# Performance work log

Measured on AMD Instinct MI355X. Metric: run time of the kernel, lower is better.

## Reference

```python
import jax, jax.numpy as jnp
import numpy as np

B, N, M, D, HEADS, L, DFF, TSTEPS = 8, 1024, 512, 128, 8, 6, 512, 100
S = N + M
HD = D // HEADS


def _layer_norm(x, g, b):
    mu = jnp.mean(x, axis=-1, keepdims=True)
    var = jnp.var(x, axis=-1, keepdims=True)
    return (x - mu) * jax.lax.rsqrt(var + 1e-5) * g + b


def setup_inputs() -> dict:
    rng = np.random.default_rng(0)
    # sparse parity-check matrix, ~6 ones per check row
    H = (rng.random((M, N)) < 6.0 / N).astype(np.float32)
    # create_mask with n_rings=1: eye(S) plus variable<->check Tanner edges
    conn = np.eye(S, dtype=np.float32)
    conn[N:, :N] = np.maximum(conn[N:, :N], H)
    conn[:N, N:] = np.maximum(conn[:N, N:], H.T)
    mask = ~(conn > 0)  # True = attention blocked (src_mask semantics)

    key = jax.random.key(0)
    ks = jax.random.split(key, 16)
    s = 0.05  # weight init scale ~ 1/sqrt(d_model)
    return {
        "r_t": jax.random.normal(ks[0], (B, N), jnp.float32),
        "t": jax.random.randint(ks[1], (B,), 0, TSTEPS),
        "pcm": jnp.asarray(H.astype(np.int32)),
        "mask": jnp.asarray(mask),
        "src_embed": jax.random.uniform(ks[2], (S, D), jnp.float32),
        "time_table": jax.random.normal(ks[3], (TSTEPS, D), jnp.float32),
        "Wq": jax.random.normal(ks[4], (L, D, D), jnp.float32) * s,
        "Wk": jax.random.normal(ks[5], (L, D, D), jnp.float32) * s,
        "Wv": jax.random.normal(ks[6], (L, D, D), jnp.float32) * s,
        "Wo": jax.random.normal(ks[7], (L, D, D), jnp.float32) * s,
        "W1": jax.random.normal(ks[8], (L, D, DFF), jnp.float32) * s,
        "W2": jax.random.normal(ks[9], (L, DFF, D), jnp.float32) * s,
        "g1": jnp.ones((L, D), jnp.float32),
        "b1": jnp.zeros((L, D), jnp.float32),
        "g2": jnp.ones((L, D), jnp.float32),
        "b2": jnp.zeros((L, D), jnp.float32),
        "fc_w": jax.random.normal(ks[10], (D, 1), jnp.float32) * s,
        "fc_b": jnp.zeros((1,), jnp.float32),
    }


def reference(r_t, t, pcm, mask, src_embed, time_table, Wq, Wk, Wv, Wo,
              W1, W2, g1, b1, g2, b2, fc_w, fc_b):
    # to_bin: BPSK sign -> bit {0,1}
    bits = 0.5 * (1.0 - jnp.sign(r_t))                       # [B, N]
    syn = (bits @ pcm.T.astype(jnp.float32)) % 2.0           # mod-2 syndrome [B, M]
    nodes = jnp.concatenate([jnp.abs(r_t), syn], axis=-1)    # [B, S]
    x = src_embed[None, :, :] * nodes[:, :, None]            # [B, S, D]
    te = time_table[t]                                       # [B, D] time embedding
    x = te[:, None, :] * x                                   # time-modulated input
    bias = jnp.where(mask, -1e9, 0.0)[None, None]            # [1, 1, S, S]
    inv_sqrt_hd = 1.0 / jnp.sqrt(jnp.float32(HD))
    for l in range(L):
        h = _layer_norm(x, g1[l], b1[l])
        q = (h @ Wq[l]).reshape(B, S, HEADS, HD)
        k = (h @ Wk[l]).reshape(B, S, HEADS, HD)
        v = (h @ Wv[l]).reshape(B, S, HEADS, HD)
        scores = jnp.einsum('bqhd,bkhd->bhqk', q, k) * inv_sqrt_hd + bias
        p = jax.nn.softmax(scores, axis=-1)
        o = jnp.einsum('bhqk,bkhd->bqhd', p, v).reshape(B, S, D)
        x = x + o @ Wo[l]
        # FiLM-style time conditioning on the FFN branch
        h2 = _layer_norm(x, g2[l], b2[l]) * te[:, None, :]
        x = x + jax.nn.relu(h2 @ W1[l]) @ W2[l]
    return x @ fc_w + fc_b                                   # z_hat [B, S, 1]
```

## Files before the change

kernel.cpp:

```cpp
#include <hip/hip_runtime.h>
#include <cmath>
#include <cstdint>

constexpr int B_ = 8, N_ = 1024, M_ = 512, D_ = 128, S_ = 1536, L_ = 6, DFF_ = 512;
constexpr int ROWS = B_ * S_;
constexpr int MAXDEG = 64;
constexpr int LKEY = 32;
constexpr int RPB  = 48;
constexpr int NBLK = ROWS / RPB;
constexpr int BPB  = S_ / RPB;
constexpr int NTILE = 12;
constexpr int TILE  = 128 * 128;

typedef __bf16 bf16x8 __attribute__((ext_vector_type(8)));
typedef float  f32x4  __attribute__((ext_vector_type(4)));
typedef unsigned short u16x8 __attribute__((ext_vector_type(8)));

__device__ inline unsigned short f2bf(float f) {
  unsigned u = __float_as_uint(f);
  u += 0x7fffu + ((u >> 16) & 1u);
  return (unsigned short)(u >> 16);
}
__device__ inline float bf2f(unsigned short u) {
  return __uint_as_float(((unsigned)u) << 16);
}
__device__ inline void ull2f4(unsigned long long u, float* f) {
  f[0] = bf2f((unsigned short)(u));
  f[1] = bf2f((unsigned short)(u >> 16));
  f[2] = bf2f((unsigned short)(u >> 32));
  f[3] = bf2f((unsigned short)(u >> 48));
}

__device__ __forceinline__ void async_ld16(const unsigned short* g, unsigned short* l) {
  __builtin_amdgcn_global_load_lds(
      (const __attribute__((address_space(1))) unsigned int*)(uintptr_t)g,
      (__attribute__((address_space(3))) unsigned int*)(unsigned)(uintptr_t)l,
      16, 0, 0);
}
__device__ __forceinline__ void issue_tile(const unsigned short* tp, unsigned short* bs,
                                           int w, int lane) {
  for (int c = w; c < 32; c += 6)
    async_ld16(tp + c * 512 + lane * 8, bs + c * 512);
}

__global__ void adj_init(int* __restrict__ adj, int* __restrict__ adjcnt) {
  int s = blockIdx.x * blockDim.x + threadIdx.x;
  if (s < S_) { adj[s * MAXDEG] = s; adjcnt[s] = 1; }
}
__global__ void adj_build(const int* __restrict__ pcm, int* __restrict__ adj,
                          int* __restrict__ adjcnt) {
  int c = blockIdx.x;
  int lane = threadIdx.x;
  const int* row = pcm + c * N_;
  for (int base = 0; base < N_; base += 64) {
    int k = base + lane;
    if (row[k] != 0) {
      int s1 = atomicAdd(&adjcnt[N_ + c], 1);
      if (s1 < MAXDEG) adj[(N_ + c) * MAXDEG + s1] = k;
      int s2 = atomicAdd(&adjcnt[k], 1);
      if (s2 < MAXDEG) adj[k * MAXDEG + s2] = N_ + c;
    }
  }
}

__global__ void xinit_kernel(const float* __restrict__ r_t, const int* __restrict__ adj,
                             const int* __restrict__ adjcnt, const float* __restrict__ se,
                             const int* __restrict__ tt, const float* __restrict__ table,
                             float* __restrict__ x, unsigned* __restrict__ barrier_cnt) {
  int bs = blockIdx.x;
  int b = bs / S_, s = bs % S_;
  int d = threadIdx.x;
  if (bs < 8 && d == 0)
    __hip_atomic_store(barrier_cnt + bs * 32, 0u, __ATOMIC_RELAXED, __HIP_MEMORY_SCOPE_AGENT);
  float node;
  if (s < N_) {
    node = fabsf(r_t[b * N_ + s]);
  } else {
    int cnt = adjcnt[s]; cnt = cnt < MAXDEG ? cnt : MAXDEG;
    float sum = 0.f;
    for (int j = 0; j < cnt; ++j) {
      int k = adj[s * MAXDEG + j];
      if (k < N_) {
        float r = r_t[b * N_ + k];
        sum += (r < 0.f) ? 1.f : (r > 0.f ? 0.f : 0.5f);
      }
    }
    node = fmodf(sum, 2.0f);
  }
  x[(size_t)bs * D_ + d] = table[tt[b] * D_ + d] * se[s * D_ + d] * node;
}

constexpr int WLAYER = NTILE * TILE;

__global__ void wconv_kernel(const float* __restrict__ Wq, const float* __restrict__ Wk,
                             const float* __restrict__ Wv, const float* __restrict__ Wo,
                             const float* __restrict__ W1, const float* __restrict__ W2,
                             unsigned short* __restrict__ out) {
  __shared__ unsigned short tl[128 * 130];
  int bid = blockIdx.x;
  int l = bid / NTILE, tile = bid % NTILE;
  const float* src;
  int rstride, coff = 0;
  if (tile == 0)      { src = Wk + (size_t)l * D_ * D_;  rstride = D_; }
  else if (tile == 1) { src = Wv + (size_t)l * D_ * D_;  rstride = D_; }
  else if (tile == 2) { src = Wq + (size_t)l * D_ * D_;  rstride = D_; }
  else if (tile == 3) { src = Wo + (size_t)l * D_ * D_;  rstride = D_; }
  else {
    int c = (tile - 4) >> 1;
    if (((tile - 4) & 1) == 0) { src = W1 + (size_t)l * D_ * DFF_; rstride = DFF_; coff = c * 128; }
    else                       { src = W2 + (size_t)l * DFF_ * D_ + (size_t)c * 128 * D_; rstride = D_; }
  }
  for (int i = threadIdx.x; i < 16384; i += 256) {
    int kd = i >> 7, rr = i & 127;
    tl[kd * 130 + rr] = f2bf(src[(size_t)kd * rstride + coff + rr]);
  }
  __syncthreads();
  unsigned short* o = out + (size_t)bid * TILE;
  for (int i = threadIdx.x; i < 16384; i += 256) {
    int rr = i >> 7;
    int sw = (i >> 3) & 15, e = i & 7;
    int kd = (sw ^ (rr & 15)) * 8 + e;
    o[i] = tl[kd * 130 + rr];
  }
}

__device__ __forceinline__ void mfma4(const unsigned short* As, const unsigned short* Bs,
                                      int rowbase, int colbase, int quad, int l16,
                                      f32x4 (&acc)[4]) {
#pragma unroll
  for (int kk = 0; kk < 4; ++kk) {
    int cb = kk * 4 + quad;
    int row = rowbase + l16;
    bf16x8 a = __builtin_bit_cast(bf16x8, *(const uint4*)&As[row * 128 + ((cb ^ (row & 15)) << 3)]);
    bf16x8 bb[4];
#pragma unroll
    for (int ct = 0; ct < 4; ++ct) {
      int n = colbase + ct * 16 + l16;
      bb[ct] = __builtin_bit_cast(bf16x8, *(const uint4*)&Bs[n * 128 + ((cb ^ (n & 15)) << 3)]);
    }
#pragma unroll
    for (int ct = 0; ct < 4; ++ct)
      acc[ct] = __builtin_amdgcn_mfma_f32_16x16x32_bf16(a, bb[ct], acc[ct], 0, 0, 0);
  }
}

__device__ __forceinline__ void grid_barrier(unsigned* cnt, unsigned target) {
  __syncthreads();
  if (threadIdx.x == 0) {
    __hip_atomic_fetch_add(cnt, 1u, __ATOMIC_RELAXED, __HIP_MEMORY_SCOPE_AGENT);
    while (__hip_atomic_load(cnt, __ATOMIC_RELAXED, __HIP_MEMORY_SCOPE_AGENT) < target)
      __builtin_amdgcn_s_sleep(4);
  }
  __syncthreads();
}

__global__ void __launch_bounds__(384) mega_kernel(
    const float* __restrict__ x0, unsigned short* __restrict__ kv0,
    unsigned short* __restrict__ kv1, const unsigned short* __restrict__ wbf,
    const float* __restrict__ g1, const float* __restrict__ b1,
    const float* __restrict__ g2, const float* __restrict__ b2,
    const int* __restrict__ tt, const float* __restrict__ table,
    const int* __restrict__ adj, const int* __restrict__ adjc,
    const float* __restrict__ fcw, const float* __restrict__ fcb,
    float* __restrict__ out, unsigned* barrier_cnt) {
  __shared__ unsigned short As[RPB * 128];
  __shared__ unsigned short Bs[2][TILE];
  __shared__ unsigned short Cs[RPB * 128];
  __shared__ unsigned short KVs[RPB * 256];
  __shared__ float red1[2][RPB], red2[2][RPB];
  __shared__ int sKeys[RPB * LKEY];
  __shared__ int sCnt[RPB];
  const int row0 = blockIdx.x * RPB;
  const int b = row0 / S_;
  const int bS = b * S_;
  const int t = threadIdx.x, w = t >> 6, lane = t & 63, quad = lane >> 4, l16 = lane & 15;
  const int wr = w >> 1, wc = w & 1;
  const int rowbase = wr * 16, colbase = wc * 64;
  const int tbase = tt[b] * D_;
  unsigned* bcnt = barrier_cnt + b * 32;

  issue_tile(wbf, Bs[0], w, lane);

  f32x4 xreg[4];
#pragma unroll
  for (int ct = 0; ct < 4; ++ct)
#pragma unroll
    for (int i = 0; i < 4; ++i) {
      int row = row0 + rowbase + quad * 4 + i;
      int col = colbase + ct * 16 + l16;
      xreg[ct][i] = x0[(size_t)row * D_ + col];
    }
  if (t < RPB) {
    int c = adjc[row0 + t - bS];
    sCnt[t] = c < MAXDEG ? c : MAXDEG;
  }
  for (int i = t; i < RPB * LKEY; i += 384) {
    int r = i / LKEY, j = i % LKEY;
    sKeys[i] = adj[(row0 + r - bS) * MAXDEG + j];
  }

  for (int l = 0; l < L_; ++l) {
    const unsigned short* wt = wbf + (size_t)l * WLAYER;
    const float* g1l = g1 + l * D_;
    const float* b1l = b1 + l * D_;
    const float* g2l = g2 + l * D_;
    const float* b2l = b2 + l * D_;
    unsigned short* kv = (l & 1) ? kv1 : kv0;

    float mu1[4], rs1[4];
#pragma unroll
    for (int i = 0; i < 4; ++i) {
      float s = xreg[0][i] + xreg[1][i] + xreg[2][i] + xreg[3][i];
      for (int off = 1; off < 16; off <<= 1) s += __shfl_xor(s, off);
      if (l16 == 0) red1[wc][rowbase + quad * 4 + i] = s;
    }
    __syncthreads();
#pragma unroll
    for (int i = 0; i < 4; ++i) {
      int r = rowbase + quad * 4 + i;
      mu1[i] = (red1[0][r] + red1[1][r]) * (1.f / 128.f);
      float sq = 0.f;
#pragma unroll
      for (int ct = 0; ct < 4; ++ct) { float d = xreg[ct][i] - mu1[i]; sq += d * d; }
      for (int off = 1; off < 16; off <<= 1) sq += __shfl_xor(sq, off);
      if (l16 == 0) red2[wc][r] = sq;
    }
    __syncthreads();
#pragma unroll
    for (int i = 0; i < 4; ++i) {
      int r = rowbase + quad * 4 + i;
      rs1[i] = rsqrtf((red2[0][r] + red2[1][r]) * (1.f / 128.f) + 1e-5f);
    }
#pragma unroll
    for (int ct = 0; ct < 4; ++ct)
#pragma unroll
      for (int i = 0; i < 4; ++i) {
        int rowL = rowbase + quad * 4 + i;
        int col = colbase + ct * 16 + l16;
        float h = (xreg[ct][i] - mu1[i]) * rs1[i] * g1l[col] + b1l[col];
        As[rowL * 128 + (((col >> 3) ^ (rowL & 15)) << 3) + (col & 7)] = f2bf(h);
      }
    __syncthreads();

    issue_tile(wt + 1 * TILE, Bs[1], w, lane);
    {
      f32x4 acc[4];
#pragma unroll
      for (int j = 0; j < 4; ++j) acc[j] = f32x4{0.f, 0.f, 0.f, 0.f};
      mfma4(As, Bs[0], rowbase, colbase, quad, l16, acc);
#pragma unroll
      for (int ct = 0; ct < 4; ++ct)
#pragma unroll
        for (int i = 0; i < 4; ++i) {
          int rowL = rowbase + quad * 4 + i;
          KVs[rowL * 256 + colbase + ct * 16 + l16] = f2bf(acc[ct][i]);
        }
    }
    __syncthreads();
    issue_tile(wt + 2 * TILE, Bs[0], w, lane);
    {
      f32x4 acc[4];
#pragma unroll
      for (int j = 0; j < 4; ++j) acc[j] = f32x4{0.f, 0.f, 0.f, 0.f};
      mfma4(As, Bs[1], rowbase, colbase, quad, l16, acc);
#pragma unroll
      for (int ct = 0; ct < 4; ++ct)
#pragma unroll
        for (int i = 0; i < 4; ++i) {
          int rowL = rowbase + quad * 4 + i;
          KVs[rowL * 256 + 128 + colbase + ct * 16 + l16] = f2bf(acc[ct][i]);
        }
    }
    __syncthreads();
    issue_tile(wt + 3 * TILE, Bs[1], w, lane);
    {
      f32x4 acc[4];
#pragma unroll
      for (int j = 0; j < 4; ++j) acc[j] = f32x4{0.f, 0.f, 0.f, 0.f};
      mfma4(As, Bs[0], rowbase, colbase, quad, l16, acc);
#pragma unroll
      for (int ct = 0; ct < 4; ++ct)
#pragma unroll
        for (int i = 0; i < 4; ++i) {
          int rowL = rowbase + quad * 4 + i;
          int col = colbase + ct * 16 + l16;
          Cs[rowL * 128 + (((col >> 3) ^ (rowL & 15)) << 3) + (col & 7)] = f2bf(acc[ct][i]);
        }
    }
    for (int i = t; i < RPB * 128; i += 384) {
      int rL = i >> 7, cw = i & 127;
      unsigned u = *(const unsigned*)&KVs[rL * 256 + cw * 2];
      __hip_atomic_store((unsigned*)&kv[(size_t)(row0 + rL) * 256 + cw * 2],
                         u, __ATOMIC_RELAXED, __HIP_MEMORY_SCOPE_AGENT);
    }

    grid_barrier(bcnt, (unsigned)(BPB * (l + 1)));

    issue_tile(wt + 4 * TILE, Bs[0], w, lane);

    {
      const int rL = t >> 3, h = t & 7;
      const int s = row0 + rL - bS;
      const int cnt = sCnt[rL];
      float q[16];
      {
        u16x8 qa = *(const u16x8*)&Cs[rL * 128 + (((2 * h) ^ (rL & 15)) << 3)];
        u16x8 qb = *(const u16x8*)&Cs[rL * 128 + (((2 * h + 1) ^ (rL & 15)) << 3)];
#pragma unroll
        for (int j = 0; j < 8; ++j) { q[j] = bf2f(qa[j]); q[8 + j] = bf2f(qb[j]); }
      }
      float m = -1e30f, lsum = 0.f;
      float o16[16];
#pragma unroll
      for (int j = 0; j < 16; ++j) o16[j] = 0.f;
      for (int jb = 0; jb < cnt; jb += 4) {
        unsigned long long K[4][4], V[4][4];
#pragma unroll
        for (int u = 0; u < 4; ++u) {
          int j = jb + u;
          int key = 0;
          if (j < cnt) key = (j < LKEY) ? sKeys[rL * LKEY + j] : adj[s * MAXDEG + j];
          const unsigned long long* kp =
              (const unsigned long long*)(kv + (size_t)(bS + key) * 256 + h * 16);
#pragma unroll
          for (int c = 0; c < 4; ++c) {
            K[u][c] = __hip_atomic_load(kp + c, __ATOMIC_RELAXED, __HIP_MEMORY_SCOPE_AGENT);
            V[u][c] = __hip_atomic_load(kp + 32 + c, __ATOMIC_RELAXED, __HIP_MEMORY_SCOPE_AGENT);
          }
        }
#pragma unroll
        for (int u = 0; u < 4; ++u) {
          float kf[16], vf[16];
#pragma unroll
          for (int c = 0; c < 4; ++c) { ull2f4(K[u][c], kf + 4 * c); ull2f4(V[u][c], vf + 4 * c); }
          float dot = 0.f;
#pragma unroll
          for (int j = 0; j < 16; ++j) dot = fmaf(q[j], kf[j], dot);
          dot *= 0.25f;
          if (jb + u >= cnt) dot = -1e30f;
          const float mn = fmaxf(m, dot);
          const float rescale = __expf(m - mn);
          const float e = __expf(dot - mn);
          lsum = lsum * rescale + e;
#pragma unroll
          for (int j = 0; j < 16; ++j) o16[j] = o16[j] * rescale + e * vf[j];
          m = mn;
        }
      }
      const float inv = 1.f / lsum;
      u16x8 pk0, pk1;
#pragma unroll
      for (int j = 0; j < 8; ++j) {
        pk0[j] = f2bf(o16[j] * inv);
        pk1[j] = f2bf(o16[8 + j] * inv);
      }
      *(u16x8*)&As[rL * 128 + (((2 * h) ^ (rL & 15)) << 3)] = pk0;
      *(u16x8*)&As[rL * 128 + (((2 * h + 1) ^ (rL & 15)) << 3)] = pk1;
    }
    __syncthreads();

    f32x4 acc1[4];
#pragma unroll
    for (int j = 0; j < 4; ++j) acc1[j] = f32x4{0.f, 0.f, 0.f, 0.f};
    mfma4(As, Bs[1], rowbase, colbase, quad, l16, acc1);
    f32x4 xp[4];
#pragma unroll
    for (int ct = 0; ct < 4; ++ct)
#pragma unroll
      for (int i = 0; i < 4; ++i) xp[ct][i] = xreg[ct][i] + acc1[ct][i];
#pragma unroll
    for (int i = 0; i < 4; ++i) {
      float s = xp[0][i] + xp[1][i] + xp[2][i] + xp[3][i];
      for (int off = 1; off < 16; off <<= 1) s += __shfl_xor(s, off);
      if (l16 == 0) red1[wc][rowbase + quad * 4 + i] = s;
    }
    __syncthreads();
    float mu_[4], rs_[4];
#pragma unroll
    for (int i = 0; i < 4; ++i) {
      int r = rowbase + quad * 4 + i;
      mu_[i] = (red1[0][r] + red1[1][r]) * (1.f / 128.f);
      float sq = 0.f;
#pragma unroll
      for (int ct = 0; ct < 4; ++ct) { float d = xp[ct][i] - mu_[i]; sq += d * d; }
      for (int off = 1; off < 16; off <<= 1) sq += __shfl_xor(sq, off);
      if (l16 == 0) red2[wc][r] = sq;
    }
    __syncthreads();
#pragma unroll
    for (int i = 0; i < 4; ++i) {
      int r = rowbase + quad * 4 + i;
      rs_[i] = rsqrtf((red2[0][r] + red2[1][r]) * (1.f / 128.f) + 1e-5f);
    }
#pragma unroll
    for (int ct = 0; ct < 4; ++ct)
#pragma unroll
      for (int i = 0; i < 4; ++i) {
        int rowL = rowbase + quad * 4 + i;
        int col = colbase + ct * 16 + l16;
        float h2 = (xp[ct][i] - mu_[i]) * rs_[i] * g2l[col] + b2l[col];
        h2 *= table[tbase + col];
        As[rowL * 128 + (((col >> 3) ^ (rowL & 15)) << 3) + (col & 7)] = f2bf(h2);
      }
    __syncthreads();

    f32x4 acc2[4];
#pragma unroll
    for (int j = 0; j < 4; ++j) acc2[j] = f32x4{0.f, 0.f, 0.f, 0.f};
    for (int c = 0; c < 4; ++c) {
      issue_tile(wt + (5 + 2 * c) * TILE, Bs[1], w, lane);
      f32x4 accF[4];
#pragma unroll
      for (int j = 0; j < 4; ++j) accF[j] = f32x4{0.f, 0.f, 0.f, 0.f};
      mfma4(As, Bs[0], rowbase, colbase, quad, l16, accF);
#pragma unroll
      for (int ct = 0; ct < 4; ++ct)
#pragma unroll
        for (int i = 0; i < 4; ++i) {
          int rowL = rowbase + quad * 4 + i;
          int col = colbase + ct * 16 + l16;
          Cs[rowL * 128 + (((col >> 3) ^ (rowL & 15)) << 3) + (col & 7)] =
              f2bf(fmaxf(accF[ct][i], 0.f));
        }
      __syncthreads();
      if (c < 3) issue_tile(wt + (6 + 2 * c) * TILE, Bs[0], w, lane);
      else if (l < L_ - 1) issue_tile(wt + WLAYER, Bs[0], w, lane);
      mfma4(Cs, Bs[1], rowbase, colbase, quad, l16, acc2);
      __syncthreads();
    }
    if (l < L_ - 1) {
#pragma unroll
      for (int ct = 0; ct < 4; ++ct)
#pragma unroll
        for (int i = 0; i < 4; ++i) xreg[ct][i] = xp[ct][i] + acc2[ct][i];
    } else {
      float pr[4] = {0.f, 0.f, 0.f, 0.f};
#pragma unroll
      for (int ct = 0; ct < 4; ++ct)
#pragma unroll
        for (int i = 0; i < 4; ++i)
          pr[i] += (xp[ct][i] + acc2[ct][i]) * fcw[colbase + ct * 16 + l16];
#pragma unroll
      for (int i = 0; i < 4; ++i) {
        float s = pr[i];
        for (int off = 1; off < 16; off <<= 1) s += __shfl_xor(s, off);
        if (l16 == 0) red1[wc][rowbase + quad * 4 + i] = s;
      }
      __syncthreads();
      if (wc == 0 && l16 == 0)
#pragma unroll
        for (int i = 0; i < 4; ++i) {
          int r = rowbase + quad * 4 + i;
          out[row0 + r] = red1[0][r] + red1[1][r] + fcb[0];
        }
    }
  }
}

extern "C" void kernel_launch(void* const* d_in, const int* in_sizes, int n_in,
                              void* d_out, int out_size, void* d_ws, size_t ws_size,
                              hipStream_t stream) {
  const float* r_t       = (const float*)d_in[0];
  const int*   t         = (const int*)d_in[1];
  const int*   pcm       = (const int*)d_in[2];
  const float* src_embed = (const float*)d_in[4];
  const float* time_tab  = (const float*)d_in[5];
  const float* Wq = (const float*)d_in[6];
  const float* Wk = (const float*)d_in[7];
  const float* Wv = (const float*)d_in[8];
  const float* Wo = (const float*)d_in[9];
  const float* W1 = (const float*)d_in[10];
  const float* W2 = (const float*)d_in[11];
  const float* g1 = (const float*)d_in[12];
  const float* b1 = (const float*)d_in[13];
  const float* g2 = (const float*)d_in[14];
  const float* b2 = (const float*)d_in[15];
  const float* fc_w = (const float*)d_in[16];
  const float* fc_b = (const float*)d_in[17];
  float* out = (float*)d_out;

  char* ws = (char*)d_ws;
  size_t off = 0;
  auto alloc = [&](size_t bytes) -> void* {
    void* p = ws + off;
    off = (off + bytes + 255) & ~(size_t)255;
    return p;
  };
  float*          x    = (float*)alloc((size_t)ROWS * D_ * 4);
  unsigned short* kv0  = (unsigned short*)alloc((size_t)ROWS * 256 * 2);
  unsigned short* kv1  = (unsigned short*)alloc((size_t)ROWS * 256 * 2);
  int*            adj  = (int*)alloc((size_t)S_ * MAXDEG * 4);
  int*            adjc = (int*)alloc((size_t)S_ * 4);
  unsigned short* wbf  = (unsigned short*)alloc((size_t)L_ * WLAYER * 2);
  unsigned*       bcnt = (unsigned*)alloc(8 * 32 * 4);

  adj_init<<<(S_ + 255) / 256, 256, 0, stream>>>(adj, adjc);
  adj_build<<<M_, 64, 0, stream>>>(pcm, adj, adjc);
  wconv_kernel<<<L_ * NTILE, 256, 0, stream>>>(Wq, Wk, Wv, Wo, W1, W2, wbf);
  xinit_kernel<<<ROWS, 128, 0, stream>>>(r_t, adj, adjc, src_embed, t, time_tab, x, bcnt);

  mega_kernel<<<NBLK, 384, 0, stream>>>(x, kv0, kv1, wbf, g1, b1, g2, b2,
                                        t, time_tab, adj, adjc, fc_w, fc_b, out, bcnt);
}
```

Measured before the change: 290.3 us.

## Triple-buffer weight tiles and fuse layernorm mean/variance reductions

```diff
diff --git a/kernel.cpp b/kernel.cpp
--- a/kernel.cpp
+++ b/kernel.cpp
@@ -164,7 +164,7 @@
     const float* __restrict__ fcw, const float* __restrict__ fcb,
     float* __restrict__ out, unsigned* barrier_cnt) {
   __shared__ unsigned short As[RPB * 128];
-  __shared__ unsigned short Bs[2][TILE];
+  __shared__ unsigned short Bs[3][TILE];
   __shared__ unsigned short Cs[RPB * 128];
   __shared__ unsigned short KVs[RPB * 256];
   __shared__ float red1[2][RPB], red2[2][RPB];
@@ -179,7 +179,9 @@
   const int tbase = tt[b] * D_;
   unsigned* bcnt = barrier_cnt + b * 32;
 
-  issue_tile(wbf, Bs[0], w, lane);
+  issue_tile(wbf + 0 * TILE, Bs[0], w, lane);
+  issue_tile(wbf + 1 * TILE, Bs[1], w, lane);
+  issue_tile(wbf + 2 * TILE, Bs[2], w, lane);
 
   f32x4 xreg[4];
 #pragma unroll
@@ -210,26 +212,20 @@
     float mu1[4], rs1[4];
 #pragma unroll
     for (int i = 0; i < 4; ++i) {
-      float s = xreg[0][i] + xreg[1][i] + xreg[2][i] + xreg[3][i];
-      for (int off = 1; off < 16; off <<= 1) s += __shfl_xor(s, off);
-      if (l16 == 0) red1[wc][rowbase + quad * 4 + i] = s;
+      float s = 0.f, sq = 0.f;
+#pragma unroll
+      for (int ct = 0; ct < 4; ++ct) { s += xreg[ct][i]; sq += xreg[ct][i] * xreg[ct][i]; }
+      for (int off = 1; off < 16; off <<= 1) { s += __shfl_xor(s, off); sq += __shfl_xor(sq, off); }
+      if (l16 == 0) { red1[wc][rowbase + quad * 4 + i] = s; red2[wc][rowbase + quad * 4 + i] = sq; }
     }
     __syncthreads();
 #pragma unroll
     for (int i = 0; i < 4; ++i) {
       int r = rowbase + quad * 4 + i;
-      mu1[i] = (red1[0][r] + red1[1][r]) * (1.f / 128.f);
-      float sq = 0.f;
-#pragma unroll
-      for (int ct = 0; ct < 4; ++ct) { float d = xreg[ct][i] - mu1[i]; sq += d * d; }
-      for (int off = 1; off < 16; off <<= 1) sq += __shfl_xor(sq, off);
-      if (l16 == 0) red2[wc][r] = sq;
-    }
-    __syncthreads();
-#pragma unroll
-    for (int i = 0; i < 4; ++i) {
-      int r = rowbase + quad * 4 + i;
-      rs1[i] = rsqrtf((red2[0][r] + red2[1][r]) * (1.f / 128.f) + 1e-5f);
+      float mu = (red1[0][r] + red1[1][r]) * (1.f / 128.f);
+      float var = (red2[0][r] + red2[1][r]) * (1.f / 128.f) - mu * mu;
+      mu1[i] = mu;
+      rs1[i] = rsqrtf(var + 1e-5f);
     }
 #pragma unroll
     for (int ct = 0; ct < 4; ++ct)
@@ -242,7 +238,6 @@
       }
     __syncthreads();
 
-    issue_tile(wt + 1 * TILE, Bs[1], w, lane);
     {
       f32x4 acc[4];
 #pragma unroll
@@ -256,8 +251,6 @@
           KVs[rowL * 256 + colbase + ct * 16 + l16] = f2bf(acc[ct][i]);
         }
     }
-    __syncthreads();
-    issue_tile(wt + 2 * TILE, Bs[0], w, lane);
     {
       f32x4 acc[4];
 #pragma unroll
@@ -271,13 +264,11 @@
           KVs[rowL * 256 + 128 + colbase + ct * 16 + l16] = f2bf(acc[ct][i]);
         }
     }
-    __syncthreads();
-    issue_tile(wt + 3 * TILE, Bs[1], w, lane);
     {
       f32x4 acc[4];
 #pragma unroll
       for (int j = 0; j < 4; ++j) acc[j] = f32x4{0.f, 0.f, 0.f, 0.f};
-      mfma4(As, Bs[0], rowbase, colbase, quad, l16, acc);
+      mfma4(As, Bs[2], rowbase, colbase, quad, l16, acc);
 #pragma unroll
       for (int ct = 0; ct < 4; ++ct)
 #pragma unroll
@@ -287,6 +278,7 @@
           Cs[rowL * 128 + (((col >> 3) ^ (rowL & 15)) << 3) + (col & 7)] = f2bf(acc[ct][i]);
         }
     }
+    __syncthreads();
     for (int i = t; i < RPB * 128; i += 384) {
       int rL = i >> 7, cw = i & 127;
       unsigned u = *(const unsigned*)&KVs[rL * 256 + cw * 2];
@@ -296,7 +288,9 @@
 
     grid_barrier(bcnt, (unsigned)(BPB * (l + 1)));
 
-    issue_tile(wt + 4 * TILE, Bs[0], w, lane);
+    issue_tile(wt + 3 * TILE, Bs[0], w, lane);
+    issue_tile(wt + 4 * TILE, Bs[1], w, lane);
+    issue_tile(wt + 5 * TILE, Bs[2], w, lane);
 
     {
       const int rL = t >> 3, h = t & 7;
@@ -362,35 +356,29 @@
     f32x4 acc1[4];
 #pragma unroll
     for (int j = 0; j < 4; ++j) acc1[j] = f32x4{0.f, 0.f, 0.f, 0.f};
-    mfma4(As, Bs[1], rowbase, colbase, quad, l16, acc1);
+    mfma4(As, Bs[0], rowbase, colbase, quad, l16, acc1);
     f32x4 xp[4];
 #pragma unroll
     for (int ct = 0; ct < 4; ++ct)
 #pragma unroll
       for (int i = 0; i < 4; ++i) xp[ct][i] = xreg[ct][i] + acc1[ct][i];
+    float mu_[4], rs_[4];
 #pragma unroll
     for (int i = 0; i < 4; ++i) {
-      float s = xp[0][i] + xp[1][i] + xp[2][i] + xp[3][i];
-      for (int off = 1; off < 16; off <<= 1) s += __shfl_xor(s, off);
-      if (l16 == 0) red1[wc][rowbase + quad * 4 + i] = s;
-    }
-    __syncthreads();
-    float mu_[4], rs_[4];
+      float s = 0.f, sq = 0.f;
+#pragma unroll
+      for (int ct = 0; ct < 4; ++ct) { s += xp[ct][i]; sq += xp[ct][i] * xp[ct][i]; }
+      for (int off = 1; off < 16; off <<= 1) { s += __shfl_xor(s, off); sq += __shfl_xor(sq, off); }
+      if (l16 == 0) { red1[wc][rowbase + quad * 4 + i] = s; red2[wc][rowbase + quad * 4 + i] = sq; }
+    }
+    __syncthreads();
 #pragma unroll
     for (int i = 0; i < 4; ++i) {
       int r = rowbase + quad * 4 + i;
-      mu_[i] = (red1[0][r] + red1[1][r]) * (1.f / 128.f);
-      float sq = 0.f;
-#pragma unroll
-      for (int ct = 0; ct < 4; ++ct) { float d = xp[ct][i] - mu_[i]; sq += d * d; }
-      for (int off = 1; off < 16; off <<= 1) sq += __shfl_xor(sq, off);
-      if (l16 == 0) red2[wc][r] = sq;
-    }
-    __syncthreads();
-#pragma unroll
-    for (int i = 0; i < 4; ++i) {
-      int r = rowbase + quad * 4 + i;
-      rs_[i] = rsqrtf((red2[0][r] + red2[1][r]) * (1.f / 128.f) + 1e-5f);
+      float mu = (red1[0][r] + red1[1][r]) * (1.f / 128.f);
+      float var = (red2[0][r] + red2[1][r]) * (1.f / 128.f) - mu * mu;
+      mu_[i] = mu;
+      rs_[i] = rsqrtf(var + 1e-5f);
     }
 #pragma unroll
     for (int ct = 0; ct < 4; ++ct)
@@ -407,12 +395,14 @@
     f32x4 acc2[4];
 #pragma unroll
     for (int j = 0; j < 4; ++j) acc2[j] = f32x4{0.f, 0.f, 0.f, 0.f};
+    const int bufW1[4] = {1, 0, 2, 1};
+    const int bufW2[4] = {2, 1, 0, 2};
+#pragma unroll
     for (int c = 0; c < 4; ++c) {
-      issue_tile(wt + (5 + 2 * c) * TILE, Bs[1], w, lane);
       f32x4 accF[4];
 #pragma unroll
       for (int j = 0; j < 4; ++j) accF[j] = f32x4{0.f, 0.f, 0.f, 0.f};
-      mfma4(As, Bs[0], rowbase, colbase, quad, l16, accF);
+      mfma4(As, Bs[bufW1[c]], rowbase, colbase, quad, l16, accF);
 #pragma unroll
       for (int ct = 0; ct < 4; ++ct)
 #pragma unroll
@@ -423,10 +413,15 @@
               f2bf(fmaxf(accF[ct][i], 0.f));
         }
       __syncthreads();
-      if (c < 3) issue_tile(wt + (6 + 2 * c) * TILE, Bs[0], w, lane);
-      else if (l < L_ - 1) issue_tile(wt + WLAYER, Bs[0], w, lane);
-      mfma4(Cs, Bs[1], rowbase, colbase, quad, l16, acc2);
+      if (c < 3) issue_tile(wt + (4 + 2 * (c + 1)) * TILE, Bs[bufW1[c + 1]], w, lane);
+      else if (l < L_ - 1) issue_tile(wt + WLAYER + 0 * TILE, Bs[0], w, lane);
+      mfma4(Cs, Bs[bufW2[c]], rowbase, colbase, quad, l16, acc2);
       __syncthreads();
+      if (c < 3) issue_tile(wt + (5 + 2 * (c + 1)) * TILE, Bs[bufW2[c + 1]], w, lane);
+      else if (l < L_ - 1) {
+        issue_tile(wt + WLAYER + 1 * TILE, Bs[1], w, lane);
+        issue_tile(wt + WLAYER + 2 * TILE, Bs[2], w, lane);
+      }
     }
     if (l < L_ - 1) {
 #pragma unroll
```

Result: no change. 286.6 us (-1.3%).
